# Performance work log

Hardware: AMD Instinct MI355X
Metric: run time of the kernel (lower is better)

The kernel has to match this reference:

```python
import jax, jax.numpy as jnp
import numpy as np

TEMPERATURE = 8.0  # sqrt(d_head=64)
CLAMP = 15.0
EPS = 1e-6


def setup_inputs() -> dict:
    key = jax.random.key(0)
    kq, kk, kv, km = jax.random.split(key, 4)
    B, Lq, Lk, D = 16, 2048, 2048, 64
    q = jax.random.normal(kq, (B, Lq, D), dtype=jnp.float32)
    k = jax.random.normal(kk, (B, Lk, D), dtype=jnp.float32)
    v = jax.random.normal(kv, (B, Lk, D), dtype=jnp.float32)
    mask = jax.random.randint(km, (B, Lq, Lk), 0, 2).astype(jnp.float32)
    return {"q": q, "k": k, "v": v, "mask": mask}


def masked_softmax(x, m, axis=-1):
    # clamp -> multiply by mask -> stable exp -> multiply by mask -> normalize
    x = jnp.clip(x, -CLAMP, CLAMP)
    x = x * m
    e_x = jnp.exp(x - jnp.max(x, axis=axis, keepdims=True))
    e_x = e_x * m
    return e_x / (jnp.sum(e_x, axis=axis, keepdims=True) + EPS)


def reference(q, k, v, mask):
    # scores: [B, Lq, Lk]
    attn = jnp.einsum('bqd,bkd->bqk', q, k) / TEMPERATURE
    attn = masked_softmax(attn, mask, axis=2)
    # dropout is identity in eval mode (deterministic reference)
    output = jnp.einsum('bqk,bkd->bqd', attn, v)
    return (output, attn)
```

## Files before the change

kernel.cpp:

```cpp
#include <hip/hip_runtime.h>
#include <stdint.h>

#define NB 16
#define LQ 2048
#define LK 2048
#define DH 64
#define QT 16
#define NW 16
#define STRIP (NW * 16)
#define NIT (LK / STRIP)

typedef short bf16x8 __attribute__((ext_vector_type(8)));
typedef float f32x4 __attribute__((ext_vector_type(4)));

__device__ __forceinline__ unsigned short f2bf(float f) {
    union { float f; uint32_t u; } v; v.f = f;
    uint32_t u = v.u;
    u += 0x7FFFu + ((u >> 16) & 1u);
    return (unsigned short)(u >> 16);
}
__device__ __forceinline__ float bf2f(unsigned short h) {
    union { uint32_t u; float f; } v; v.u = ((uint32_t)h) << 16;
    return v.f;
}
__device__ __forceinline__ uint32_t pack2(float lo, float hi) {
    return (uint32_t)f2bf(lo) | ((uint32_t)f2bf(hi) << 16);
}

__global__ void convert_kernel(const float* __restrict__ q, const float* __restrict__ k,
                               const float* __restrict__ v,
                               unsigned short* __restrict__ qb,
                               unsigned short* __restrict__ kb,
                               unsigned short* __restrict__ vtb) {
    int bid = blockIdx.x;
    int tid = threadIdx.x;
    if (bid < 2048) {
        const float* src = (bid < 1024) ? q : k;
        unsigned short* dst = (bid < 1024) ? qb : kb;
        int64_t off = (int64_t)(bid & 1023) * 2048 + (int64_t)tid * 8;
        float4 a = *(const float4*)(src + off);
        float4 b4 = *(const float4*)(src + off + 4);
        uint4 o;
        o.x = pack2(a.x, a.y);
        o.y = pack2(a.z, a.w);
        o.z = pack2(b4.x, b4.y);
        o.w = pack2(b4.z, b4.w);
        *(uint4*)(dst + off) = o;
    } else {
        __shared__ unsigned short tile[64][72];
        int bid2 = bid - 2048;
        int bb = bid2 >> 5, kt = bid2 & 31;
        int k0 = kt * 64;
        int krow = tid >> 2, dc = (tid & 3) * 16;
        const float* vp = v + ((int64_t)(bb * LK) + k0 + krow) * DH + dc;
        float4 x0 = *(const float4*)(vp);
        float4 x1 = *(const float4*)(vp + 4);
        float4 x2 = *(const float4*)(vp + 8);
        float4 x3 = *(const float4*)(vp + 12);
        float vals[16] = {x0.x, x0.y, x0.z, x0.w, x1.x, x1.y, x1.z, x1.w,
                          x2.x, x2.y, x2.z, x2.w, x3.x, x3.y, x3.z, x3.w};
        #pragma unroll
        for (int i = 0; i < 16; ++i) tile[dc + i][krow] = f2bf(vals[i]);
        __syncthreads();
        int d = tid >> 2, kc = (tid & 3) * 16;
        uint4 r0 = *(const uint4*)&tile[d][kc];
        uint4 r1 = *(const uint4*)&tile[d][kc + 8];
        unsigned short* op = vtb + ((int64_t)(bb * DH) + d) * LK + k0 + kc;
        *(uint4*)op = r0;
        *(uint4*)(op + 8) = r1;
    }
}

__launch_bounds__(1024, 8)
__global__ void attn_kernel(const unsigned short* __restrict__ qb,
                            const unsigned short* __restrict__ kb,
                            const unsigned short* __restrict__ vtb,
                            const float* __restrict__ mask,
                            float* __restrict__ out, float* __restrict__ attn) {
    extern __shared__ char smem[];
    float* denom_part = (float*)(smem + QT * LK * 2);
    float* pp         = (float*)(smem + QT * LK * 2 + 1024);

    int bid = blockIdx.x;
    int swz = (bid & 7) * 256 + (bid >> 3);
    int b = swz >> 7;
    int q0 = (swz & 127) * QT;

    int tid = threadIdx.x;
    int lane = tid & 63;
    int wave = tid >> 6;
    int lr = lane & 15, lg = lane >> 4;

    bf16x8 qf0, qf1;
    {
        const unsigned short* qp = qb + ((int64_t)(b * LQ + q0 + lr)) * DH + 8 * lg;
        qf0 = *(const bf16x8*)qp;
        qf1 = *(const bf16x8*)(qp + 32);
    }

    float dsum = 0.f;

    {
        const unsigned short* kpw =
            kb + (int64_t)b * LK * DH + (wave * 16 + lr) * DH + 8 * lg;
        const float* mrow =
            mask + ((int64_t)(b * LQ + q0 + lr)) * LK + wave * 16 + lg * 4;
        float4 mf = *(const float4*)mrow;
        #pragma unroll
        for (int kt = 0; kt < NIT; ++kt) {
            float4 nm;
            if (kt < NIT - 1) nm = *(const float4*)(mrow + (kt + 1) * STRIP);
            bf16x8 kf0 = *(const bf16x8*)(kpw + (int64_t)kt * STRIP * DH);
            bf16x8 kf1 = *(const bf16x8*)(kpw + (int64_t)kt * STRIP * DH + 32);
            f32x4 acc = {0.f, 0.f, 0.f, 0.f};
            acc = __builtin_amdgcn_mfma_f32_16x16x32_bf16(kf0, qf0, acc, 0, 0, 0);
            acc = __builtin_amdgcn_mfma_f32_16x16x32_bf16(kf1, qf1, acc, 0, 0, 0);
            float mv[4] = {mf.x, mf.y, mf.z, mf.w};
            unsigned short eb[4];
            #pragma unroll
            for (int j = 0; j < 4; ++j) {
                float s = acc[j] * 0.125f;
                s = fminf(fmaxf(s, -15.0f), 15.0f);
                float e = __expf(s * mv[j]) * mv[j];
                eb[j] = f2bf(e);
                dsum += bf2f(eb[j]);
            }
            uint2 u;
            u.x = (uint32_t)eb[0] | ((uint32_t)eb[1] << 16);
            u.y = (uint32_t)eb[2] | ((uint32_t)eb[3] << 16);
            int c = kt * STRIP + wave * 16 + lg * 4;
            int byteoff = (lr * 4096 + c * 2) ^ ((lr & 7) << 4);
            *(uint2*)(smem + byteoff) = u;
            mf = nm;
        }
    }

    {
        float s = dsum;
        s += __shfl_xor(s, 16);
        s += __shfl_xor(s, 32);
        if (lg == 0) denom_part[wave * 16 + lr] = s;
    }
    __syncthreads();

    f32x4 pacc = {0.f, 0.f, 0.f, 0.f};
    int cw = (wave & 3) * 16, kq = wave >> 2;
    {
        const unsigned short* vp =
            vtb + ((int64_t)(b * DH + cw + lr)) * LK + kq * 512 + 8 * lg;
        int rowbase = lr * 4096;
        int sw = (lr & 7) << 4;
        int kk0 = kq * 512;
        #pragma unroll 4
        for (int kk = 0; kk < 512; kk += 32) {
            int byteoff = (rowbase + (kk0 + kk + 8 * lg) * 2) ^ sw;
            bf16x8 ef = *(const bf16x8*)(smem + byteoff);
            bf16x8 vf = *(const bf16x8*)(vp + kk);
            pacc = __builtin_amdgcn_mfma_f32_16x16x32_bf16(ef, vf, pacc, 0, 0, 0);
        }
    }
    if (kq != 0) {
        #pragma unroll
        for (int j = 0; j < 4; ++j)
            pp[((kq - 1) * 4 + (wave & 3)) * 256 + (lg * 4 + j) * 16 + lr] = pacc[j];
    }
    __syncthreads();
    if (kq == 0) {
        int c4 = wave & 3;
        #pragma unroll
        for (int j = 0; j < 4; ++j) {
            int r = lg * 4 + j;
            float den = 1e-6f;
            #pragma unroll
            for (int w = 0; w < NW; ++w) den += denom_part[w * 16 + r];
            float val = pacc[j] + pp[(c4)*256 + r * 16 + lr] +
                        pp[(4 + c4) * 256 + r * 16 + lr] +
                        pp[(8 + c4) * 256 + r * 16 + lr];
            out[((int64_t)(b * LQ + q0 + r)) * DH + cw + lr] = val / den;
        }
    }

    {
        int r = tid >> 6;
        float den = 1e-6f;
        #pragma unroll
        for (int w = 0; w < NW; ++w) den += denom_part[w * 16 + r];
        float inv = 1.0f / den;
        float* ap = attn + ((int64_t)(b * LQ + q0 + r)) * LK;
        int rowbase = r * 4096;
        int sw = (r & 7) << 4;
        #pragma unroll
        for (int c0 = (tid & 63) * 8; c0 < LK; c0 += 512) {
            int byteoff = (rowbase + c0 * 2) ^ sw;
            bf16x8 ev = *(const bf16x8*)(smem + byteoff);
            float4 o0, o1;
            o0.x = bf2f((unsigned short)ev[0]) * inv;
            o0.y = bf2f((unsigned short)ev[1]) * inv;
            o0.z = bf2f((unsigned short)ev[2]) * inv;
            o0.w = bf2f((unsigned short)ev[3]) * inv;
            o1.x = bf2f((unsigned short)ev[4]) * inv;
            o1.y = bf2f((unsigned short)ev[5]) * inv;
            o1.z = bf2f((unsigned short)ev[6]) * inv;
            o1.w = bf2f((unsigned short)ev[7]) * inv;
            *(float4*)(ap + c0) = o0;
            *(float4*)(ap + c0 + 4) = o1;
        }
    }
}

extern "C" void kernel_launch(void* const* d_in, const int* in_sizes, int n_in,
                              void* d_out, int out_size, void* d_ws, size_t ws_size,
                              hipStream_t stream) {
    const float* q    = (const float*)d_in[0];
    const float* k    = (const float*)d_in[1];
    const float* v    = (const float*)d_in[2];
    const float* mask = (const float*)d_in[3];
    float* out  = (float*)d_out;
    float* attn = out + (int64_t)NB * LQ * DH;

    unsigned short* qb  = (unsigned short*)d_ws;
    unsigned short* kb  = qb + (int64_t)NB * LQ * DH;
    unsigned short* vtb = kb + (int64_t)NB * LK * DH;

    (void)hipFuncSetAttribute((const void*)attn_kernel,
                              hipFuncAttributeMaxDynamicSharedMemorySize, 78848);

    convert_kernel<<<2560, 256, 0, stream>>>(q, k, v, qb, kb, vtb);
    attn_kernel<<<2048, 1024, 78848, stream>>>(qb, kb, vtb, mask, out, attn);
}
```

Measured before the change: 230.8 us.

## Move mask application into a row-wise pass fused with attention-probability stores

The QK^T loop no longer reads the mask. It computes unmasked exp scores into shared memory and prefetches the next K fragments instead. A separate per-row pass, one wave per query row, then reads the mask with coalesced loads, zeroes masked entries, computes the denominator with a wave shuffle reduction, writes the masked values back to LDS for the PV step, and emits normalized attn rows with nontemporal stores. This removes the strided mask gathers inside the MFMA loop and the separate cross-wave denominator gather. The trade-off is an extra barrier and LDS round-trip, and the mask is now treated as a boolean select, which matches the multiply only for 0/1 masks.

```diff
diff --git a/kernel.cpp b/kernel.cpp
--- a/kernel.cpp
+++ b/kernel.cpp
@@ -79,7 +79,7 @@
                             float* __restrict__ out, float* __restrict__ attn) {
     extern __shared__ char smem[];
     float* denom_part = (float*)(smem + QT * LK * 2);
-    float* pp         = (float*)(smem + QT * LK * 2 + 1024);
+    float* pp         = (float*)(smem + QT * LK * 2 + 64);
 
     int bid = blockIdx.x;
     int swz = (bid & 7) * 256 + (bid >> 3);
@@ -98,32 +98,28 @@
         qf1 = *(const bf16x8*)(qp + 32);
     }
 
-    float dsum = 0.f;
-
     {
         const unsigned short* kpw =
             kb + (int64_t)b * LK * DH + (wave * 16 + lr) * DH + 8 * lg;
-        const float* mrow =
-            mask + ((int64_t)(b * LQ + q0 + lr)) * LK + wave * 16 + lg * 4;
-        float4 mf = *(const float4*)mrow;
+        bf16x8 kf0 = *(const bf16x8*)kpw;
+        bf16x8 kf1 = *(const bf16x8*)(kpw + 32);
         #pragma unroll
         for (int kt = 0; kt < NIT; ++kt) {
-            float4 nm;
-            if (kt < NIT - 1) nm = *(const float4*)(mrow + (kt + 1) * STRIP);
-            bf16x8 kf0 = *(const bf16x8*)(kpw + (int64_t)kt * STRIP * DH);
-            bf16x8 kf1 = *(const bf16x8*)(kpw + (int64_t)kt * STRIP * DH + 32);
+            bf16x8 nk0, nk1;
+            if (kt < NIT - 1) {
+                const unsigned short* np = kpw + (int64_t)(kt + 1) * STRIP * DH;
+                nk0 = *(const bf16x8*)np;
+                nk1 = *(const bf16x8*)(np + 32);
+            }
             f32x4 acc = {0.f, 0.f, 0.f, 0.f};
             acc = __builtin_amdgcn_mfma_f32_16x16x32_bf16(kf0, qf0, acc, 0, 0, 0);
             acc = __builtin_amdgcn_mfma_f32_16x16x32_bf16(kf1, qf1, acc, 0, 0, 0);
-            float mv[4] = {mf.x, mf.y, mf.z, mf.w};
             unsigned short eb[4];
             #pragma unroll
             for (int j = 0; j < 4; ++j) {
                 float s = acc[j] * 0.125f;
                 s = fminf(fmaxf(s, -15.0f), 15.0f);
-                float e = __expf(s * mv[j]) * mv[j];
-                eb[j] = f2bf(e);
-                dsum += bf2f(eb[j]);
+                eb[j] = f2bf(__expf(s));
             }
             uint2 u;
             u.x = (uint32_t)eb[0] | ((uint32_t)eb[1] << 16);
@@ -131,15 +127,76 @@
             int c = kt * STRIP + wave * 16 + lg * 4;
             int byteoff = (lr * 4096 + c * 2) ^ ((lr & 7) << 4);
             *(uint2*)(smem + byteoff) = u;
-            mf = nm;
-        }
-    }
-
-    {
-        float s = dsum;
-        s += __shfl_xor(s, 16);
-        s += __shfl_xor(s, 32);
-        if (lg == 0) denom_part[wave * 16 + lr] = s;
+            kf0 = nk0; kf1 = nk1;
+        }
+    }
+    __syncthreads();
+
+    {
+        int r = wave;
+        int rowbase = r * 4096;
+        int sw = (r & 7) << 4;
+        int c0l = lane * 8;
+        const float* mrow = mask + ((int64_t)(b * LQ + q0 + r)) * LK;
+
+        float4 mk[8];
+        #pragma unroll
+        for (int i = 0; i < 4; ++i) {
+            mk[2 * i]     = *(const float4*)(mrow + i * 512 + c0l);
+            mk[2 * i + 1] = *(const float4*)(mrow + i * 512 + c0l + 4);
+        }
+        bf16x8 pv[4];
+        #pragma unroll
+        for (int i = 0; i < 4; ++i) {
+            int byteoff = (rowbase + (i * 512 + c0l) * 2) ^ sw;
+            pv[i] = *(const bf16x8*)(smem + byteoff);
+        }
+        float dsum = 0.f;
+        uint32_t esave[16];
+        #pragma unroll
+        for (int i = 0; i < 4; ++i) {
+            float mv[8] = {mk[2 * i].x, mk[2 * i].y, mk[2 * i].z, mk[2 * i].w,
+                           mk[2 * i + 1].x, mk[2 * i + 1].y, mk[2 * i + 1].z,
+                           mk[2 * i + 1].w};
+            uint32_t packed[4];
+            #pragma unroll
+            for (int h = 0; h < 4; ++h) {
+                unsigned short p0 = (unsigned short)pv[i][2 * h];
+                unsigned short p1 = (unsigned short)pv[i][2 * h + 1];
+                unsigned short e0 = (mv[2 * h] != 0.f) ? p0 : (unsigned short)0;
+                unsigned short e1 = (mv[2 * h + 1] != 0.f) ? p1 : (unsigned short)0;
+                dsum += bf2f(e0) + bf2f(e1);
+                packed[h] = (uint32_t)e0 | ((uint32_t)e1 << 16);
+                esave[i * 4 + h] = packed[h];
+            }
+            uint4 wb = {packed[0], packed[1], packed[2], packed[3]};
+            int byteoff = (rowbase + (i * 512 + c0l) * 2) ^ sw;
+            *(uint4*)(smem + byteoff) = wb;
+        }
+        dsum += __shfl_xor(dsum, 1);
+        dsum += __shfl_xor(dsum, 2);
+        dsum += __shfl_xor(dsum, 4);
+        dsum += __shfl_xor(dsum, 8);
+        dsum += __shfl_xor(dsum, 16);
+        dsum += __shfl_xor(dsum, 32);
+        float den = dsum + 1e-6f;
+        if (lane == 0) denom_part[r] = den;
+        float inv = 1.0f / den;
+        float* ap = attn + ((int64_t)(b * LQ + q0 + r)) * LK;
+        #pragma unroll
+        for (int i = 0; i < 4; ++i) {
+            f32x4 o0, o1;
+            o0[0] = bf2f((unsigned short)(esave[i * 4 + 0] & 0xffff)) * inv;
+            o0[1] = bf2f((unsigned short)(esave[i * 4 + 0] >> 16)) * inv;
+            o0[2] = bf2f((unsigned short)(esave[i * 4 + 1] & 0xffff)) * inv;
+            o0[3] = bf2f((unsigned short)(esave[i * 4 + 1] >> 16)) * inv;
+            o1[0] = bf2f((unsigned short)(esave[i * 4 + 2] & 0xffff)) * inv;
+            o1[1] = bf2f((unsigned short)(esave[i * 4 + 2] >> 16)) * inv;
+            o1[2] = bf2f((unsigned short)(esave[i * 4 + 3] & 0xffff)) * inv;
+            o1[3] = bf2f((unsigned short)(esave[i * 4 + 3] >> 16)) * inv;
+            __builtin_nontemporal_store(o0, (f32x4*)(ap + i * 512 + c0l));
+            __builtin_nontemporal_store(o1, (f32x4*)(ap + i * 512 + c0l + 4));
+        }
     }
     __syncthreads();
 
@@ -170,40 +227,11 @@
         #pragma unroll
         for (int j = 0; j < 4; ++j) {
             int r = lg * 4 + j;
-            float den = 1e-6f;
-            #pragma unroll
-            for (int w = 0; w < NW; ++w) den += denom_part[w * 16 + r];
-            float val = pacc[j] + pp[(c4)*256 + r * 16 + lr] +
+            float den = denom_part[r];
+            float val = pacc[j] + pp[(c4) * 256 + r * 16 + lr] +
                         pp[(4 + c4) * 256 + r * 16 + lr] +
                         pp[(8 + c4) * 256 + r * 16 + lr];
             out[((int64_t)(b * LQ + q0 + r)) * DH + cw + lr] = val / den;
-        }
-    }
-
-    {
-        int r = tid >> 6;
-        float den = 1e-6f;
-        #pragma unroll
-        for (int w = 0; w < NW; ++w) den += denom_part[w * 16 + r];
-        float inv = 1.0f / den;
-        float* ap = attn + ((int64_t)(b * LQ + q0 + r)) * LK;
-        int rowbase = r * 4096;
-        int sw = (r & 7) << 4;
-        #pragma unroll
-        for (int c0 = (tid & 63) * 8; c0 < LK; c0 += 512) {
-            int byteoff = (rowbase + c0 * 2) ^ sw;
-            bf16x8 ev = *(const bf16x8*)(smem + byteoff);
-            float4 o0, o1;
-            o0.x = bf2f((unsigned short)ev[0]) * inv;
-            o0.y = bf2f((unsigned short)ev[1]) * inv;
-            o0.z = bf2f((unsigned short)ev[2]) * inv;
-            o0.w = bf2f((unsigned short)ev[3]) * inv;
-            o1.x = bf2f((unsigned short)ev[4]) * inv;
-            o1.y = bf2f((unsigned short)ev[5]) * inv;
-            o1.z = bf2f((unsigned short)ev[6]) * inv;
-            o1.w = bf2f((unsigned short)ev[7]) * inv;
-            *(float4*)(ap + c0) = o0;
-            *(float4*)(ap + c0 + 4) = o1;
         }
     }
 }
@@ -223,8 +251,8 @@
     unsigned short* vtb = kb + (int64_t)NB * LK * DH;
 
     (void)hipFuncSetAttribute((const void*)attn_kernel,
-                              hipFuncAttributeMaxDynamicSharedMemorySize, 78848);
+                              hipFuncAttributeMaxDynamicSharedMemorySize, 77888);
 
     convert_kernel<<<2560, 256, 0, stream>>>(q, k, v, qb, kb, vtb);
-    attn_kernel<<<2048, 1024, 78848, stream>>>(qb, kb, vtb, mask, out, attn);
-}
+    attn_kernel<<<2048, 1024, 77888, stream>>>(qb, kb, vtb, mask, out, attn);
+}
```

Result: faster. 209.7 us (-9.1%).

## Reorder attn store before PV, deepen prefetch, use nontemporal stores

Applied to the files above, without the earlier changes.

The attention-probability writeback now runs before the PV MMA phase instead of after it, so the large fp32 attn stores can overlap with the PV compute and V loads. The row denominator is computed once and kept in shared memory for the output stage. The QK loop prefetches K fragments one tile ahead and mask values two tiles ahead. The masked exp becomes a select instead of a multiply. The attn stores use nontemporal hints to avoid polluting the cache. This costs extra registers for the prefetch buffers and slightly more shared memory.

```diff
diff --git a/kernel.cpp b/kernel.cpp
--- a/kernel.cpp
+++ b/kernel.cpp
@@ -79,7 +79,8 @@
                             float* __restrict__ out, float* __restrict__ attn) {
     extern __shared__ char smem[];
     float* denom_part = (float*)(smem + QT * LK * 2);
-    float* pp         = (float*)(smem + QT * LK * 2 + 1024);
+    float* denF       = (float*)(smem + QT * LK * 2 + 1024);
+    float* pp         = (float*)(smem + QT * LK * 2 + 1088);
 
     int bid = blockIdx.x;
     int swz = (bid & 7) * 256 + (bid >> 3);
@@ -105,24 +106,31 @@
             kb + (int64_t)b * LK * DH + (wave * 16 + lr) * DH + 8 * lg;
         const float* mrow =
             mask + ((int64_t)(b * LQ + q0 + lr)) * LK + wave * 16 + lg * 4;
-        float4 mf = *(const float4*)mrow;
+        bf16x8 kf0 = *(const bf16x8*)kpw;
+        bf16x8 kf1 = *(const bf16x8*)(kpw + 32);
+        float4 mcur = *(const float4*)mrow;
+        float4 mn1  = *(const float4*)(mrow + STRIP);
         #pragma unroll
         for (int kt = 0; kt < NIT; ++kt) {
-            float4 nm;
-            if (kt < NIT - 1) nm = *(const float4*)(mrow + (kt + 1) * STRIP);
-            bf16x8 kf0 = *(const bf16x8*)(kpw + (int64_t)kt * STRIP * DH);
-            bf16x8 kf1 = *(const bf16x8*)(kpw + (int64_t)kt * STRIP * DH + 32);
+            float4 mn2;
+            if (kt + 2 < NIT) mn2 = *(const float4*)(mrow + (kt + 2) * STRIP);
+            bf16x8 nk0, nk1;
+            if (kt + 1 < NIT) {
+                const unsigned short* np = kpw + (int64_t)(kt + 1) * STRIP * DH;
+                nk0 = *(const bf16x8*)np;
+                nk1 = *(const bf16x8*)(np + 32);
+            }
             f32x4 acc = {0.f, 0.f, 0.f, 0.f};
             acc = __builtin_amdgcn_mfma_f32_16x16x32_bf16(kf0, qf0, acc, 0, 0, 0);
             acc = __builtin_amdgcn_mfma_f32_16x16x32_bf16(kf1, qf1, acc, 0, 0, 0);
-            float mv[4] = {mf.x, mf.y, mf.z, mf.w};
+            float mv[4] = {mcur.x, mcur.y, mcur.z, mcur.w};
             unsigned short eb[4];
             #pragma unroll
             for (int j = 0; j < 4; ++j) {
                 float s = acc[j] * 0.125f;
                 s = fminf(fmaxf(s, -15.0f), 15.0f);
-                float e = __expf(s * mv[j]) * mv[j];
-                eb[j] = f2bf(e);
+                unsigned short p = f2bf(__expf(s));
+                eb[j] = (mv[j] != 0.f) ? p : (unsigned short)0;
                 dsum += bf2f(eb[j]);
             }
             uint2 u;
@@ -131,17 +139,44 @@
             int c = kt * STRIP + wave * 16 + lg * 4;
             int byteoff = (lr * 4096 + c * 2) ^ ((lr & 7) << 4);
             *(uint2*)(smem + byteoff) = u;
-            mf = nm;
-        }
-    }
-
-    {
-        float s = dsum;
-        s += __shfl_xor(s, 16);
-        s += __shfl_xor(s, 32);
-        if (lg == 0) denom_part[wave * 16 + lr] = s;
-    }
+            kf0 = nk0; kf1 = nk1;
+            mcur = mn1; mn1 = mn2;
+        }
+    }
+
+    dsum += __shfl_xor(dsum, 16);
+    dsum += __shfl_xor(dsum, 32);
+    if (lane < 16) denom_part[wave * 16 + lane] = dsum;
     __syncthreads();
+
+    {
+        int r = wave;
+        float den = 1e-6f;
+        #pragma unroll
+        for (int w = 0; w < NW; ++w) den += denom_part[w * 16 + r];
+        if (lane == 0) denF[r] = den;
+        float inv = 1.0f / den;
+        float* ap = attn + ((int64_t)(b * LQ + q0 + r)) * LK;
+        int rowbase = r * 4096;
+        int sw = (r & 7) << 4;
+        int c0l = lane * 8;
+        #pragma unroll
+        for (int i = 0; i < 4; ++i) {
+            int byteoff = (rowbase + (i * 512 + c0l) * 2) ^ sw;
+            bf16x8 ev = *(const bf16x8*)(smem + byteoff);
+            f32x4 o0, o1;
+            o0[0] = bf2f((unsigned short)ev[0]) * inv;
+            o0[1] = bf2f((unsigned short)ev[1]) * inv;
+            o0[2] = bf2f((unsigned short)ev[2]) * inv;
+            o0[3] = bf2f((unsigned short)ev[3]) * inv;
+            o1[0] = bf2f((unsigned short)ev[4]) * inv;
+            o1[1] = bf2f((unsigned short)ev[5]) * inv;
+            o1[2] = bf2f((unsigned short)ev[6]) * inv;
+            o1[3] = bf2f((unsigned short)ev[7]) * inv;
+            __builtin_nontemporal_store(o0, (f32x4*)(ap + i * 512 + c0l));
+            __builtin_nontemporal_store(o1, (f32x4*)(ap + i * 512 + c0l + 4));
+        }
+    }
 
     f32x4 pacc = {0.f, 0.f, 0.f, 0.f};
     int cw = (wave & 3) * 16, kq = wave >> 2;
@@ -170,40 +205,11 @@
         #pragma unroll
         for (int j = 0; j < 4; ++j) {
             int r = lg * 4 + j;
-            float den = 1e-6f;
-            #pragma unroll
-            for (int w = 0; w < NW; ++w) den += denom_part[w * 16 + r];
-            float val = pacc[j] + pp[(c4)*256 + r * 16 + lr] +
+            float den = denF[r];
+            float val = pacc[j] + pp[(c4) * 256 + r * 16 + lr] +
                         pp[(4 + c4) * 256 + r * 16 + lr] +
                         pp[(8 + c4) * 256 + r * 16 + lr];
             out[((int64_t)(b * LQ + q0 + r)) * DH + cw + lr] = val / den;
-        }
-    }
-
-    {
-        int r = tid >> 6;
-        float den = 1e-6f;
-        #pragma unroll
-        for (int w = 0; w < NW; ++w) den += denom_part[w * 16 + r];
-        float inv = 1.0f / den;
-        float* ap = attn + ((int64_t)(b * LQ + q0 + r)) * LK;
-        int rowbase = r * 4096;
-        int sw = (r & 7) << 4;
-        #pragma unroll
-        for (int c0 = (tid & 63) * 8; c0 < LK; c0 += 512) {
-            int byteoff = (rowbase + c0 * 2) ^ sw;
-            bf16x8 ev = *(const bf16x8*)(smem + byteoff);
-            float4 o0, o1;
-            o0.x = bf2f((unsigned short)ev[0]) * inv;
-            o0.y = bf2f((unsigned short)ev[1]) * inv;
-            o0.z = bf2f((unsigned short)ev[2]) * inv;
-            o0.w = bf2f((unsigned short)ev[3]) * inv;
-            o1.x = bf2f((unsigned short)ev[4]) * inv;
-            o1.y = bf2f((unsigned short)ev[5]) * inv;
-            o1.z = bf2f((unsigned short)ev[6]) * inv;
-            o1.w = bf2f((unsigned short)ev[7]) * inv;
-            *(float4*)(ap + c0) = o0;
-            *(float4*)(ap + c0 + 4) = o1;
         }
     }
 }
@@ -223,8 +229,8 @@
     unsigned short* vtb = kb + (int64_t)NB * LK * DH;
 
     (void)hipFuncSetAttribute((const void*)attn_kernel,
-                              hipFuncAttributeMaxDynamicSharedMemorySize, 78848);
+                              hipFuncAttributeMaxDynamicSharedMemorySize, 78912);
 
     convert_kernel<<<2560, 256, 0, stream>>>(q, k, v, qb, kb, vtb);
-    attn_kernel<<<2048, 1024, 78848, stream>>>(qb, kb, vtb, mask, out, attn);
-}
+    attn_kernel<<<2048, 1024, 78912, stream>>>(qb, kb, vtb, mask, out, attn);
+}
```

Result: no change. 227.9 us (-1.2%).
